# Kernel tuning notes

Hardware: AMD Instinct MI355X
Metric: run time of the kernel (lower is better)

Reference implementation:

```python
import jax, jax.numpy as jnp
import numpy as np

B, D = 4096, 128
LU, LI = 10, 20
NU, NI = 100000, 100000
NFU, NFI = 2000, 5000
MARGIN = 1.0


def setup_inputs() -> dict:
    key = jax.random.key(0)
    ks = jax.random.split(key, 32)
    s = 0.05
    n = lambda i, shape: (jax.random.normal(ks[i], shape, dtype=jnp.float32) * s)
    inp = {
        'user_indices': jax.random.randint(ks[0], (B,), 0, NU),
        'user_feat': jax.random.randint(ks[1], (B, LU), 0, NFU),
        'pos_item_indices': jax.random.randint(ks[2], (B,), 0, NI),
        'pos_item_feat': jax.random.randint(ks[3], (B, LI), 0, NFI),
        'neg_item_indices': jax.random.randint(ks[4], (B, 1), 0, NI),
        'neg_item_feat': jax.random.randint(ks[5], (B, 1, LI), 0, NFI),
        'comp_neg_indices': jax.random.randint(ks[6], (B,), 0, NI),
        'eps': jax.random.normal(ks[7], (B, D), dtype=jnp.float32),
        # learned parameters
        'emb_user': n(8, (NU, D)),
        'emb_item': n(9, (NI, D)),
        'emb_feat_user': n(10, (NFU, D)).at[0].set(0.0),  # row 0 is padding
        'emb_feat_item': n(11, (NFI, D)).at[0].set(0.0),
        'pop_emb_user': n(12, (D,)),
        'int_emb_user': n(13, (D,)),
        'pop_emb_item': n(14, (D,)),
        'int_emb_item': n(15, (D,)),
        'W_pop': n(16, (D, D)), 'b_pop': jnp.zeros((D,), jnp.float32),
        'W_int': n(17, (D, D)), 'b_int': jnp.zeros((D,), jnp.float32),
        'enc_W': n(18, (LI * D, D)), 'enc_b': jnp.zeros((D,), jnp.float32),
        'dec_W': n(19, (D, LI * D)), 'dec_b': jnp.zeros((LI * D,), jnp.float32),
        'fc11_W': n(20, (D, D)), 'fc11_b': jnp.zeros((D,), jnp.float32),
        'fc12_W': n(21, (D, D)), 'fc12_b': jnp.zeros((D,), jnp.float32),
    }
    return inp


def _attend_pool(fuse, feat_mask, vec, W, b):
    # fuse: [B, L+1, D], feat_mask: [B, L+1] (int, 0 = padded)
    scores = jnp.einsum('bld,d->bl', fuse, vec)
    scores = jnp.where(feat_mask == 0, -jnp.inf, scores)
    w = jax.nn.softmax(scores, axis=1)
    pooled = jnp.einsum('bld,bl->bd', fuse, w)
    return pooled @ W + b


def _branch(idx, feat, emb_table, feat_table, pop_vec, int_vec, W_pop, b_pop, W_int, b_int):
    e = emb_table[idx]                       # [B, D]
    fe = feat_table[feat]                    # [B, L, D]
    fuse = jnp.concatenate([e[:, None, :], fe], axis=1)           # [B, L+1, D]
    ones = jnp.ones((idx.shape[0], 1), dtype=feat.dtype)
    mask = jnp.concatenate([ones, feat], axis=1)                  # [B, L+1]
    hot = _attend_pool(fuse, mask, pop_vec, W_pop, b_pop)
    cold = _attend_pool(fuse, mask, int_vec, W_int, b_int)
    return hot, cold, e, fe


def reference(user_indices, user_feat, pos_item_indices, pos_item_feat,
              neg_item_indices, neg_item_feat, comp_neg_indices, eps,
              emb_user, emb_item, emb_feat_user, emb_feat_item,
              pop_emb_user, int_emb_user, pop_emb_item, int_emb_item,
              W_pop, b_pop, W_int, b_int,
              enc_W, enc_b, dec_W, dec_b, fc11_W, fc11_b, fc12_W, fc12_b):
    neg_item_indices = neg_item_indices.squeeze(1)
    neg_item_feat = neg_item_feat.squeeze(1)

    u_hot, u_cold, _, _ = _branch(user_indices, user_feat, emb_user, emb_feat_user,
                                  pop_emb_user, int_emb_user, W_pop, b_pop, W_int, b_int)
    p_hot, p_cold, pos_e, pos_fe = _branch(pos_item_indices, pos_item_feat, emb_item, emb_feat_item,
                                           pop_emb_item, int_emb_item, W_pop, b_pop, W_int, b_int)
    n_hot, n_cold, _, _ = _branch(neg_item_indices, neg_item_feat, emb_item, emb_feat_item,
                                  pop_emb_item, int_emb_item, W_pop, b_pop, W_int, b_int)

    loss_hot = jax.nn.relu(jnp.sum((u_hot - p_hot) ** 2, -1)
                           - jnp.sum((u_hot - n_hot) ** 2, -1) + MARGIN)
    loss_cold = jax.nn.relu(jnp.sum((u_cold - p_cold) ** 2, -1)
                            - jnp.sum((u_cold - n_cold) ** 2, -1) + MARGIN)

    # VAE over positive item feature embeddings
    x = pos_fe.reshape(pos_fe.shape[0], LI * D)
    h1 = jax.nn.relu(x @ enc_W + enc_b)
    mu = h1 @ fc11_W + fc11_b
    logvar = h1 @ fc12_W + fc12_b
    z = eps * jnp.exp(0.5 * logvar) + mu
    recon = z @ dec_W + dec_b                                    # [B, LI*D]
    mse = jnp.sum((recon - x) ** 2)
    kld = -0.5 * jnp.sum(1.0 + logvar - mu ** 2 - jnp.exp(logvar))
    vae_l = mse / LI + kld

    comp_e = emb_item[comp_neg_indices]
    mmi = -jnp.sum(jax.nn.log_sigmoid(jnp.sum(z * pos_e, 1) - jnp.sum(z * comp_e, 1)))
    item_vae_loss = mmi + vae_l + jnp.sum((z - pos_e) ** 2)

    return loss_hot, loss_cold, item_vae_loss
```

## Files before the change

kernel.cpp:

```cpp
#include <hip/hip_runtime.h>
#include <math.h>

#define BATCH 4096
#define DIM 128
#define LU 10
#define LI 20

typedef float  f32x4  __attribute__((ext_vector_type(4)));
typedef short  s16x8  __attribute__((ext_vector_type(8)));

__device__ __forceinline__ short f2bf(float x) {
    unsigned u = __float_as_uint(x);
    u += 0x7FFFu + ((u >> 16) & 1u);
    return (short)(u >> 16);
}

__global__ __launch_bounds__(256) void k_prep(
    const float* __restrict__ enc_W, const float* __restrict__ dec_W,
    const float* __restrict__ fc11_W, const float* __restrict__ fc12_W,
    const float* __restrict__ W_pop, const float* __restrict__ W_int,
    const float* __restrict__ ef_item, const float* __restrict__ ef_user,
    short* __restrict__ encWT, short* __restrict__ decWT,
    short* __restrict__ fc11WT, short* __restrict__ fc12WT,
    short* __restrict__ wpopT, short* __restrict__ wintT,
    short* __restrict__ ef16, short* __restrict__ efU16)
{
    __shared__ float tile[32][33];
    const int b = blockIdx.x;
    const int t = threadIdx.x;

    if (b < 704) {
        const float* src; short* dst; int r0, c0, src_ld, dst_ld;
        if (b < 320) {
            int tk = b % 80, tj = b / 80;
            src = enc_W; dst = encWT; r0 = tk * 32; c0 = tj * 32; src_ld = 128; dst_ld = 2560;
        } else if (b < 640) {
            int tb = b - 320; int tc = tb % 80, td = tb / 80;
            src = dec_W; dst = decWT; r0 = td * 32; c0 = tc * 32; src_ld = 2560; dst_ld = 128;
        } else if (b < 656) {
            int tb = b - 640; int tk = tb % 4, tj = tb / 4;
            src = fc11_W; dst = fc11WT; r0 = tk * 32; c0 = tj * 32; src_ld = 128; dst_ld = 128;
        } else if (b < 672) {
            int tb = b - 656; int tk = tb % 4, tj = tb / 4;
            src = fc12_W; dst = fc12WT; r0 = tk * 32; c0 = tj * 32; src_ld = 128; dst_ld = 128;
        } else if (b < 688) {
            int tb = b - 672; int tk = tb % 4, tj = tb / 4;
            src = W_pop; dst = wpopT; r0 = tk * 32; c0 = tj * 32; src_ld = 128; dst_ld = 128;
        } else {
            int tb = b - 688; int tk = tb % 4, tj = tb / 4;
            src = W_int; dst = wintT; r0 = tk * 32; c0 = tj * 32; src_ld = 128; dst_ld = 128;
        }
        for (int q = 0; q < 4; ++q) {
            int e = t + q * 256;
            int r = e >> 5, c = e & 31;
            tile[r][c] = src[(size_t)(r0 + r) * src_ld + (c0 + c)];
        }
        __syncthreads();
        for (int q = 0; q < 4; ++q) {
            int e = t + q * 256;
            int r = e >> 5, c = e & 31;
            dst[(size_t)(c0 + r) * dst_ld + (r0 + c)] = f2bf(tile[c][r]);
        }
    } else if (b < 1329) {
        int base = (b - 704) * 1024 + t * 4;
        float4 v = *(const float4*)(ef_item + base);
        short4 o;
        o.x = f2bf(v.x); o.y = f2bf(v.y); o.z = f2bf(v.z); o.w = f2bf(v.w);
        *(short4*)(ef16 + base) = o;
    } else {
        int base = (b - 1329) * 1024 + t * 4;
        float4 v = *(const float4*)(ef_user + base);
        short4 o;
        o.x = f2bf(v.x); o.y = f2bf(v.y); o.z = f2bf(v.z); o.w = f2bf(v.w);
        *(short4*)(efU16 + base) = o;
    }
}

template<int L>
__device__ __forceinline__ void pool_1p(
    const int* __restrict__ idxp, const int* __restrict__ featp,
    const float* __restrict__ etab, const unsigned short* __restrict__ ftab16,
    const float* __restrict__ vpop, const float* __restrict__ vint,
    float* __restrict__ poolH, float* __restrict__ poolC,
    int i_in, int lane)
{
    const int i = __builtin_amdgcn_readfirstlane(i_in);
    const int d = lane * 2;
    const float2 vp = *(const float2*)(vpop + d);
    const float2 vi = *(const float2*)(vint + d);

    int fidx[L];
#pragma unroll
    for (int l = 0; l < L; ++l) fidx[l] = featp[i * L + l];
    const int idx0 = idxp[i];

    const float2 e0 = *(const float2*)(etab + (size_t)idx0 * DIM + d);
    unsigned rr[L];
#pragma unroll
    for (int l = 0; l < L; ++l)
        rr[l] = *(const unsigned*)(ftab16 + (size_t)fidx[l] * DIM + d);

    unsigned mbits = 1u;
#pragma unroll
    for (int l = 0; l < L; ++l) mbits |= (fidx[l] != 0 ? 2u : 0u) << l;

    float sp[L + 1], si[L + 1];
    sp[0] = e0.x * vp.x + e0.y * vp.y;
    si[0] = e0.x * vi.x + e0.y * vi.y;
#pragma unroll
    for (int l = 0; l < L; ++l) {
        float x = __uint_as_float(rr[l] << 16);
        float y = __uint_as_float(rr[l] & 0xFFFF0000u);
        sp[l + 1] = x * vp.x + y * vp.y;
        si[l + 1] = x * vi.x + y * vi.y;
    }

#pragma unroll
    for (int l = 0; l <= L; ++l) {
        float a = sp[l], b = si[l];
        a += __shfl_xor(a, 1, 64);  b += __shfl_xor(b, 1, 64);
        a += __shfl_xor(a, 2, 64);  b += __shfl_xor(b, 2, 64);
        a += __shfl_xor(a, 4, 64);  b += __shfl_xor(b, 4, 64);
        a += __shfl_xor(a, 8, 64);  b += __shfl_xor(b, 8, 64);
        a += __shfl_xor(a, 16, 64); b += __shfl_xor(b, 16, 64);
        a += __shfl_xor(a, 32, 64); b += __shfl_xor(b, 32, 64);
        sp[l] = a; si[l] = b;
    }

    float mh = sp[0], mc = si[0];
#pragma unroll
    for (int l = 1; l <= L; ++l) {
        bool v = (mbits >> l) & 1u;
        mh = v ? fmaxf(mh, sp[l]) : mh;
        mc = v ? fmaxf(mc, si[l]) : mc;
    }
    float sh = 0.f, sc = 0.f;
#pragma unroll
    for (int l = 0; l <= L; ++l) {
        bool v = (l == 0) | ((mbits >> l) & 1u);
        float eh = v ? __expf(sp[l] - mh) : 0.f;
        float ec = v ? __expf(si[l] - mc) : 0.f;
        sp[l] = eh; si[l] = ec;
        sh += eh; sc += ec;
    }
    const float rh = 1.f / sh, rc = 1.f / sc;

    float hx = sp[0] * e0.x, hy = sp[0] * e0.y;
    float cx = si[0] * e0.x, cy = si[0] * e0.y;
#pragma unroll
    for (int l = 0; l < L; ++l) {
        float x = __uint_as_float(rr[l] << 16);
        float y = __uint_as_float(rr[l] & 0xFFFF0000u);
        hx += sp[l + 1] * x; hy += sp[l + 1] * y;
        cx += si[l + 1] * x; cy += si[l + 1] * y;
    }
    float2 oH; oH.x = hx * rh; oH.y = hy * rh;
    float2 oC; oC.x = cx * rc; oC.y = cy * rc;
    *(float2*)(poolH + (size_t)i * DIM + d) = oH;
    *(float2*)(poolC + (size_t)i * DIM + d) = oC;
}

__global__ __launch_bounds__(256) void k_AB(
    const int* __restrict__ user_idx, const int* __restrict__ user_feat,
    const int* __restrict__ pos_idx,  const int* __restrict__ pos_feat,
    const int* __restrict__ neg_idx,  const int* __restrict__ neg_feat,
    const int* __restrict__ comp_idx,
    const float* __restrict__ emb_user, const float* __restrict__ emb_item,
    const float* __restrict__ pop_u, const float* __restrict__ int_u,
    const float* __restrict__ pop_i, const float* __restrict__ int_i,
    const float* __restrict__ eps,
    const float* __restrict__ enc_b,
    const float* __restrict__ fc11_b, const float* __restrict__ fc12_b,
    const short* __restrict__ encWT,
    const short* __restrict__ fc11WT, const short* __restrict__ fc12WT,
    const short* __restrict__ ef16, const short* __restrict__ efU16,
    float* __restrict__ pooled,
    short* __restrict__ zbuf, float* __restrict__ vae_part)
{
    __shared__ int   featsL[320];
    __shared__ int   spi[16], sci[16];
    __shared__ __align__(16) short hlds[2048];
    __shared__ float sdots[4][16][3];
    __shared__ float red[256];

    const int t    = threadIdx.x;
    const int w    = t >> 6;
    const int lane = t & 63;
    const int g    = lane >> 4;
    const int q    = lane & 15;
    const size_t SEC = (size_t)BATCH * DIM;

    if (blockIdx.x >= 256) {
        const int pb = blockIdx.x - 256;
        const int br = pb % 3;
        const int i  = (pb / 3) * 4 + w;
        if (br == 0) {
            pool_1p<LU>(user_idx, user_feat, emb_user,
                        (const unsigned short*)efU16, pop_u, int_u,
                        pooled + 0 * SEC, pooled + 1 * SEC, i, lane);
        } else if (br == 1) {
            pool_1p<LI>(pos_idx, pos_feat, emb_item,
                        (const unsigned short*)ef16, pop_i, int_i,
                        pooled + 2 * SEC, pooled + 3 * SEC, i, lane);
        } else {
            pool_1p<LI>(neg_idx, neg_feat, emb_item,
                        (const unsigned short*)ef16, pop_i, int_i,
                        pooled + 4 * SEC, pooled + 5 * SEC, i, lane);
        }
        return;
    }

    const int sg = blockIdx.x;
    const int i0 = sg * 16;

    if (t < 16)      spi[t] = pos_idx[i0 + t];
    else if (t < 32) sci[t - 16] = comp_idx[i0 + t - 16];
    if (t < 256) featsL[t] = pos_feat[i0 * LI + t];
    if (t < 64)  featsL[256 + t] = pos_feat[i0 * LI + 256 + t];
    __syncthreads();

    const int j0 = w * 32 + q;
    const int j1 = j0 + 16;
    const short* bbase0 = encWT + (size_t)j0 * 2560 + g * 8;
    const short* bbase1 = encWT + (size_t)j1 * 2560 + g * 8;

    f32x4 acc0 = {0.f, 0.f, 0.f, 0.f};
    f32x4 acc1 = {0.f, 0.f, 0.f, 0.f};
    for (int l = 0; l < LI; ++l) {
        const int f = featsL[q * LI + l];
        const short* arow = ef16 + (size_t)f * DIM + g * 8;
#pragma unroll
        for (int dt = 0; dt < 4; ++dt) {
            const int koff = l * 128 + dt * 32;
            s16x8 a  = *(const s16x8*)(arow + dt * 32);
            s16x8 b0 = *(const s16x8*)(bbase0 + koff);
            s16x8 b1 = *(const s16x8*)(bbase1 + koff);
            acc0 = __builtin_amdgcn_mfma_f32_16x16x32_bf16(a, b0, acc0, 0, 0, 0);
            acc1 = __builtin_amdgcn_mfma_f32_16x16x32_bf16(a, b1, acc1, 0, 0, 0);
        }
    }

    {
        float eb0 = enc_b[j0], eb1 = enc_b[j1];
#pragma unroll
        for (int r = 0; r < 4; ++r) {
            int s = g * 4 + r;
            float h0 = acc0[r] + eb0; h0 = h0 > 0.f ? h0 : 0.f;
            float h1 = acc1[r] + eb1; h1 = h1 > 0.f ? h1 : 0.f;
            int swz = (s & 7) << 3;
            hlds[(s * 128 + j0) ^ swz] = f2bf(h0);
            hlds[(s * 128 + j1) ^ swz] = f2bf(h1);
        }
    }
    __syncthreads();

    const short* fb0_11 = fc11WT + (size_t)j0 * DIM + g * 8;
    const short* fb1_11 = fc11WT + (size_t)j1 * DIM + g * 8;
    const short* fb0_12 = fc12WT + (size_t)j0 * DIM + g * 8;
    const short* fb1_12 = fc12WT + (size_t)j1 * DIM + g * 8;

    f32x4 mu0 = {0.f,0.f,0.f,0.f}, mu1 = {0.f,0.f,0.f,0.f};
    f32x4 lv0 = {0.f,0.f,0.f,0.f}, lv1 = {0.f,0.f,0.f,0.f};
#pragma unroll
    for (int kt = 0; kt < 4; ++kt) {
        int sidx = (q * 128 + kt * 32 + g * 8) ^ ((q & 7) << 3);
        s16x8 a = *(const s16x8*)&hlds[sidx];
        s16x8 w11a = *(const s16x8*)(fb0_11 + kt * 32);
        s16x8 w11b = *(const s16x8*)(fb1_11 + kt * 32);
        s16x8 w12a = *(const s16x8*)(fb0_12 + kt * 32);
        s16x8 w12b = *(const s16x8*)(fb1_12 + kt * 32);
        mu0 = __builtin_amdgcn_mfma_f32_16x16x32_bf16(a, w11a, mu0, 0, 0, 0);
        mu1 = __builtin_amdgcn_mfma_f32_16x16x32_bf16(a, w11b, mu1, 0, 0, 0);
        lv0 = __builtin_amdgcn_mfma_f32_16x16x32_bf16(a, w12a, lv0, 0, 0, 0);
        lv1 = __builtin_amdgcn_mfma_f32_16x16x32_bf16(a, w12b, lv1, 0, 0, 0);
    }

    float b11_0 = fc11_b[j0], b11_1 = fc11_b[j1];
    float b12_0 = fc12_b[j0], b12_1 = fc12_b[j1];

    float kacc = 0.f;
#pragma unroll
    for (int r = 0; r < 4; ++r) {
        const int s = g * 4 + r;
        const int i = i0 + s;
        float m0 = mu0[r] + b11_0, m1 = mu1[r] + b11_1;
        float v0 = lv0[r] + b12_0, v1 = lv1[r] + b12_1;
        float e0 = eps[(size_t)i * DIM + j0];
        float e1 = eps[(size_t)i * DIM + j1];
        float z0 = e0 * expf(0.5f * v0) + m0;
        float z1 = e1 * expf(0.5f * v1) + m1;
        zbuf[(size_t)i * DIM + j0] = f2bf(z0);
        zbuf[(size_t)i * DIM + j1] = f2bf(z1);
        kacc += (1.f + v0 - m0 * m0 - expf(v0)) + (1.f + v1 - m1 * m1 - expf(v1));

        const size_t pb2 = (size_t)spi[s] * DIM;
        const size_t cb2 = (size_t)sci[s] * DIM;
        float pe0 = emb_item[pb2 + j0], pe1 = emb_item[pb2 + j1];
        float ce0 = emb_item[cb2 + j0], ce1 = emb_item[cb2 + j1];
        float zp = z0 * pe0 + z1 * pe1;
        float zc = z0 * ce0 + z1 * ce1;
        float d0 = z0 - pe0, d1 = z1 - pe1;
        float zq = d0 * d0 + d1 * d1;
        for (int mm = 8; mm >= 1; mm >>= 1) {
            zp += __shfl_xor(zp, mm, 64);
            zc += __shfl_xor(zc, mm, 64);
            zq += __shfl_xor(zq, mm, 64);
        }
        if (q == 0) {
            sdots[w][s][0] = zp;
            sdots[w][s][1] = zc;
            sdots[w][s][2] = zq;
        }
    }

    red[t] = -0.5f * kacc;
    __syncthreads();
    if (t < 16) {
        float zp = 0.f, zc = 0.f, zq = 0.f;
        for (int ww = 0; ww < 4; ++ww) {
            zp += sdots[ww][t][0];
            zc += sdots[ww][t][1];
            zq += sdots[ww][t][2];
        }
        float x = zp - zc;
        float ls = (x >= 0.f) ? -log1pf(expf(-x)) : (x - log1pf(expf(x)));
        red[t] += -ls + zq;
    }
    __syncthreads();
    for (int off = 128; off > 0; off >>= 1) {
        if (t < off) red[t] += red[t + off];
        __syncthreads();
    }
    if (t == 0) vae_part[sg] = red[0];
}

__global__ __launch_bounds__(256) void k_C(
    const float* __restrict__ pooled,
    const short* __restrict__ wpopT, const short* __restrict__ wintT,
    const int* __restrict__ pos_feat,
    const float* __restrict__ ef_item, const float* __restrict__ dec_b,
    const short* __restrict__ decWT, const short* __restrict__ zbuf,
    float* __restrict__ out_hot, float* __restrict__ out_cold,
    float* __restrict__ dec_part)
{
    __shared__ int   featsL[320];
    __shared__ float red[256];
    __shared__ float sArr[4][16];

    const int t    = threadIdx.x;
    const int w    = t >> 6;
    const int lane = t & 63;
    const int g    = lane >> 4;
    const int q    = lane & 15;

    if (blockIdx.x >= 2048) {
        const int i0 = (blockIdx.x - 2048) * 16;
        const int h     = w >> 1;
        const int other = (w & 1) + 1;
        const float* pu = pooled + (size_t)(0 * 2 + h) * BATCH * DIM;
        const float* po = pooled + (size_t)(other * 2 + h) * BATCH * DIM;
        const short* wT = h ? wintT : wpopT;

        s16x8 afr[4];
#pragma unroll
        for (int kt = 0; kt < 4; ++kt) {
            const size_t off = (size_t)(i0 + q) * DIM + kt * 32 + g * 8;
            f32x4 ua = *(const f32x4*)(pu + off);
            f32x4 ub = *(const f32x4*)(pu + off + 4);
            f32x4 oa = *(const f32x4*)(po + off);
            f32x4 ob = *(const f32x4*)(po + off + 4);
            s16x8 v;
            v[0] = f2bf(ua[0] - oa[0]); v[1] = f2bf(ua[1] - oa[1]);
            v[2] = f2bf(ua[2] - oa[2]); v[3] = f2bf(ua[3] - oa[3]);
            v[4] = f2bf(ub[0] - ob[0]); v[5] = f2bf(ub[1] - ob[1]);
            v[6] = f2bf(ub[2] - ob[2]); v[7] = f2bf(ub[3] - ob[3]);
            afr[kt] = v;
        }

        float sq0 = 0.f, sq1 = 0.f, sq2 = 0.f, sq3 = 0.f;
        for (int fr = 0; fr < 8; ++fr) {
            const short* bb = wT + (size_t)(fr * 16 + q) * DIM + g * 8;
            f32x4 acc = {0.f, 0.f, 0.f, 0.f};
#pragma unroll
            for (int kt = 0; kt < 4; ++kt) {
                s16x8 bfr = *(const s16x8*)(bb + kt * 32);
                acc = __builtin_amdgcn_mfma_f32_16x16x32_bf16(afr[kt], bfr, acc, 0, 0, 0);
            }
            sq0 += acc[0] * acc[0]; sq1 += acc[1] * acc[1];
            sq2 += acc[2] * acc[2]; sq3 += acc[3] * acc[3];
        }
        for (int m = 8; m >= 1; m >>= 1) {
            sq0 += __shfl_xor(sq0, m, 64);
            sq1 += __shfl_xor(sq1, m, 64);
            sq2 += __shfl_xor(sq2, m, 64);
            sq3 += __shfl_xor(sq3, m, 64);
        }
        if (q == 0) {
            sArr[w][g * 4 + 0] = sq0;
            sArr[w][g * 4 + 1] = sq1;
            sArr[w][g * 4 + 2] = sq2;
            sArr[w][g * 4 + 3] = sq3;
        }
        __syncthreads();
        if (t < 16) {
            float v = sArr[0][t] - sArr[1][t] + 1.0f;
            out_hot[i0 + t] = v > 0.f ? v : 0.f;
        } else if (t < 32) {
            int s = t - 16;
            float v = sArr[2][s] - sArr[3][s] + 1.0f;
            out_cold[i0 + s] = v > 0.f ? v : 0.f;
        }
        return;
    }

    const int db     = blockIdx.x;
    const int cchunk = db >> 8;
    const int sb     = db & 255;
    const int i0     = sb * 16;

    if (t < 256) featsL[t] = pos_feat[i0 * LI + t];
    if (t < 64)  featsL[256 + t] = pos_feat[i0 * LI + 256 + t];
    __syncthreads();

    s16x8 za[4];
#pragma unroll
    for (int kt = 0; kt < 4; ++kt)
        za[kt] = *(const s16x8*)(zbuf + (size_t)(i0 + q) * DIM + kt * 32 + g * 8);

    const int cw = cchunk * 320 + w * 80;

    s16x8 bb[5][4];
    float xs[5][4];
    float bias[5];
#pragma unroll
    for (int fp = 0; fp < 5; ++fp) {
        const int c = cw + fp * 16 + q;
        const short* bp = decWT + (size_t)c * DIM + g * 8;
#pragma unroll
        for (int kt = 0; kt < 4; ++kt)
            bb[fp][kt] = *(const s16x8*)(bp + kt * 32);
        const int l = c >> 7, dcol = c & 127;
#pragma unroll
        for (int r = 0; r < 4; ++r)
            xs[fp][r] = ef_item[(size_t)featsL[(g * 4 + r) * LI + l] * DIM + dcol];
        bias[fp] = dec_b[c];
    }

    float macc = 0.f;
#pragma unroll
    for (int fp = 0; fp < 5; ++fp) {
        f32x4 acc = {0.f, 0.f, 0.f, 0.f};
#pragma unroll
        for (int kt = 0; kt < 4; ++kt)
            acc = __builtin_amdgcn_mfma_f32_16x16x32_bf16(za[kt], bb[fp][kt], acc, 0, 0, 0);
#pragma unroll
        for (int r = 0; r < 4; ++r) {
            float dd = acc[r] + bias[fp] - xs[fp][r];
            macc += dd * dd;
        }
    }

    red[t] = macc;
    __syncthreads();
    for (int off = 128; off > 0; off >>= 1) {
        if (t < off) red[t] += red[t + off];
        __syncthreads();
    }
    if (t == 0) dec_part[db] = red[0];
}

__global__ __launch_bounds__(256) void k_E(
    const float* __restrict__ vae_part, const float* __restrict__ dec_part,
    float* __restrict__ out_scalar)
{
    __shared__ float red[256];
    const int t = threadIdx.x;
    float b3 = 0.f;
    for (int qq = t; qq < 2048; qq += 256) b3 += dec_part[qq];
    red[t] = vae_part[t] + 0.05f * b3;
    __syncthreads();
    for (int off = 128; off > 0; off >>= 1) {
        if (t < off) red[t] += red[t + off];
        __syncthreads();
    }
    if (t == 0) out_scalar[0] = red[0];
}

extern "C" void kernel_launch(void* const* d_in, const int* in_sizes, int n_in,
                              void* d_out, int out_size, void* d_ws, size_t ws_size,
                              hipStream_t stream) {
    const int*   user_idx  = (const int*)d_in[0];
    const int*   user_feat = (const int*)d_in[1];
    const int*   pos_idx   = (const int*)d_in[2];
    const int*   pos_feat  = (const int*)d_in[3];
    const int*   neg_idx   = (const int*)d_in[4];
    const int*   neg_feat  = (const int*)d_in[5];
    const int*   comp_idx  = (const int*)d_in[6];
    const float* eps       = (const float*)d_in[7];
    const float* emb_user  = (const float*)d_in[8];
    const float* emb_item  = (const float*)d_in[9];
    const float* ef_user   = (const float*)d_in[10];
    const float* ef_item   = (const float*)d_in[11];
    const float* pop_u     = (const float*)d_in[12];
    const float* int_u     = (const float*)d_in[13];
    const float* pop_i     = (const float*)d_in[14];
    const float* int_i     = (const float*)d_in[15];
    const float* W_pop     = (const float*)d_in[16];
    const float* W_int     = (const float*)d_in[18];
    const float* enc_W     = (const float*)d_in[20];
    const float* enc_b     = (const float*)d_in[21];
    const float* dec_W     = (const float*)d_in[22];
    const float* dec_b     = (const float*)d_in[23];
    const float* fc11_W    = (const float*)d_in[24];
    const float* fc11_b    = (const float*)d_in[25];
    const float* fc12_W    = (const float*)d_in[26];
    const float* fc12_b    = (const float*)d_in[27];

    float* out = (float*)d_out;
    char*  ws  = (char*)d_ws;

    short* encWT    = (short*)(ws);
    short* decWT    = (short*)(ws + 655360);
    short* fc11WT   = (short*)(ws + 1310720);
    short* fc12WT   = (short*)(ws + 1343488);
    short* wpopT    = (short*)(ws + 1376256);
    short* wintT    = (short*)(ws + 1409024);
    short* ef16     = (short*)(ws + 1441792);
    short* efU16    = (short*)(ws + 2721792);
    short* zbuf     = (short*)(ws + 3233792);
    float* pooled   = (float*)(ws + 4282368);
    float* vae_part = (float*)(ws + 16865280);
    float* dec_part = (float*)(ws + 16866304);

    k_prep<<<dim3(1579), dim3(256), 0, stream>>>(
        enc_W, dec_W, fc11_W, fc12_W, W_pop, W_int, ef_item, ef_user,
        encWT, decWT, fc11WT, fc12WT, wpopT, wintT, ef16, efU16);

    k_AB<<<dim3(3328), dim3(256), 0, stream>>>(
        user_idx, user_feat, pos_idx, pos_feat, neg_idx, neg_feat, comp_idx,
        emb_user, emb_item,
        pop_u, int_u, pop_i, int_i,
        eps, enc_b, fc11_b, fc12_b,
        encWT, fc11WT, fc12WT, ef16, efU16,
        pooled, zbuf, vae_part);

    k_C<<<dim3(2304), dim3(256), 0, stream>>>(
        pooled, wpopT, wintT, pos_feat, ef_item, dec_b, decWT, zbuf,
        out, out + BATCH, dec_part);

    k_E<<<dim3(1), dim3(256), 0, stream>>>(vae_part, dec_part, out + 2 * BATCH);
}
```

Baseline: 90.91 us.

## Precompute per-feature attention scores in prep kernel and gather them in pooling

Adds blocks to the prep kernel that compute the dot product of every feature-table row with the pop and int attention vectors and store them as scalar tables. The pooling routine then gathers these precomputed scores per feature instead of computing per-lane products followed by a 6-step shuffle reduction for each of the L+1 slots. Only the slot for the main embedding still needs the in-wave reduction. This moves the work to 7000 table rows, which is comparable to the 12288 pooled samples, and adds 875 prep blocks plus scattered scalar gathers in exchange for far fewer cross-lane shuffles.

```diff
diff --git a/kernel.cpp b/kernel.cpp
--- a/kernel.cpp
+++ b/kernel.cpp
@@ -20,10 +20,14 @@
     const float* __restrict__ fc11_W, const float* __restrict__ fc12_W,
     const float* __restrict__ W_pop, const float* __restrict__ W_int,
     const float* __restrict__ ef_item, const float* __restrict__ ef_user,
+    const float* __restrict__ pop_i, const float* __restrict__ int_i,
+    const float* __restrict__ pop_u, const float* __restrict__ int_u,
     short* __restrict__ encWT, short* __restrict__ decWT,
     short* __restrict__ fc11WT, short* __restrict__ fc12WT,
     short* __restrict__ wpopT, short* __restrict__ wintT,
-    short* __restrict__ ef16, short* __restrict__ efU16)
+    short* __restrict__ ef16, short* __restrict__ efU16,
+    float* __restrict__ projIP, float* __restrict__ projII,
+    float* __restrict__ projUP, float* __restrict__ projUI)
 {
     __shared__ float tile[32][33];
     const int b = blockIdx.x;
@@ -67,27 +71,49 @@
         short4 o;
         o.x = f2bf(v.x); o.y = f2bf(v.y); o.z = f2bf(v.z); o.w = f2bf(v.w);
         *(short4*)(ef16 + base) = o;
-    } else {
+    } else if (b < 1579) {
         int base = (b - 1329) * 1024 + t * 4;
         float4 v = *(const float4*)(ef_user + base);
         short4 o;
         o.x = f2bf(v.x); o.y = f2bf(v.y); o.z = f2bf(v.z); o.w = f2bf(v.w);
         *(short4*)(efU16 + base) = o;
+    } else {
+        const int pb = b - 1579;
+        const float* tab; const float* v0p; const float* v1p;
+        float* o0; float* o1; int row;
+        if (pb < 625) {
+            row = pb * 8 + (t >> 5);
+            tab = ef_item; v0p = pop_i; v1p = int_i; o0 = projIP; o1 = projII;
+        } else {
+            row = (pb - 625) * 8 + (t >> 5);
+            tab = ef_user; v0p = pop_u; v1p = int_u; o0 = projUP; o1 = projUI;
+        }
+        const int d = (t & 31) * 4;
+        float4 rv = *(const float4*)(tab + (size_t)row * DIM + d);
+        float4 a  = *(const float4*)(v0p + d);
+        float4 c  = *(const float4*)(v1p + d);
+        float s0 = rv.x * a.x + rv.y * a.y + rv.z * a.z + rv.w * a.w;
+        float s1 = rv.x * c.x + rv.y * c.y + rv.z * c.z + rv.w * c.w;
+        s0 += __shfl_xor(s0, 1, 64);  s1 += __shfl_xor(s1, 1, 64);
+        s0 += __shfl_xor(s0, 2, 64);  s1 += __shfl_xor(s1, 2, 64);
+        s0 += __shfl_xor(s0, 4, 64);  s1 += __shfl_xor(s1, 4, 64);
+        s0 += __shfl_xor(s0, 8, 64);  s1 += __shfl_xor(s1, 8, 64);
+        s0 += __shfl_xor(s0, 16, 64); s1 += __shfl_xor(s1, 16, 64);
+        if ((t & 31) == 0) { o0[row] = s0; o1[row] = s1; }
     }
 }
 
 template<int L>
-__device__ __forceinline__ void pool_1p(
+__device__ __forceinline__ void pool_sc(
     const int* __restrict__ idxp, const int* __restrict__ featp,
     const float* __restrict__ etab, const unsigned short* __restrict__ ftab16,
+    const float* __restrict__ projP, const float* __restrict__ projI,
     const float* __restrict__ vpop, const float* __restrict__ vint,
     float* __restrict__ poolH, float* __restrict__ poolC,
     int i_in, int lane)
 {
     const int i = __builtin_amdgcn_readfirstlane(i_in);
     const int d = lane * 2;
-    const float2 vp = *(const float2*)(vpop + d);
-    const float2 vi = *(const float2*)(vint + d);
 
     int fidx[L];
 #pragma unroll
@@ -100,32 +126,30 @@
     for (int l = 0; l < L; ++l)
         rr[l] = *(const unsigned*)(ftab16 + (size_t)fidx[l] * DIM + d);
 
+    float sp[L + 1], si[L + 1];
+#pragma unroll
+    for (int l = 0; l < L; ++l) {
+        sp[l + 1] = projP[fidx[l]];
+        si[l + 1] = projI[fidx[l]];
+    }
+
+    {
+        const float2 vp = *(const float2*)(vpop + d);
+        const float2 vi = *(const float2*)(vint + d);
+        float aH = e0.x * vp.x + e0.y * vp.y;
+        float aC = e0.x * vi.x + e0.y * vi.y;
+        aH += __shfl_xor(aH, 1, 64);  aC += __shfl_xor(aC, 1, 64);
+        aH += __shfl_xor(aH, 2, 64);  aC += __shfl_xor(aC, 2, 64);
+        aH += __shfl_xor(aH, 4, 64);  aC += __shfl_xor(aC, 4, 64);
+        aH += __shfl_xor(aH, 8, 64);  aC += __shfl_xor(aC, 8, 64);
+        aH += __shfl_xor(aH, 16, 64); aC += __shfl_xor(aC, 16, 64);
+        aH += __shfl_xor(aH, 32, 64); aC += __shfl_xor(aC, 32, 64);
+        sp[0] = aH; si[0] = aC;
+    }
+
     unsigned mbits = 1u;
 #pragma unroll
     for (int l = 0; l < L; ++l) mbits |= (fidx[l] != 0 ? 2u : 0u) << l;
-
-    float sp[L + 1], si[L + 1];
-    sp[0] = e0.x * vp.x + e0.y * vp.y;
-    si[0] = e0.x * vi.x + e0.y * vi.y;
-#pragma unroll
-    for (int l = 0; l < L; ++l) {
-        float x = __uint_as_float(rr[l] << 16);
-        float y = __uint_as_float(rr[l] & 0xFFFF0000u);
-        sp[l + 1] = x * vp.x + y * vp.y;
-        si[l + 1] = x * vi.x + y * vi.y;
-    }
-
-#pragma unroll
-    for (int l = 0; l <= L; ++l) {
-        float a = sp[l], b = si[l];
-        a += __shfl_xor(a, 1, 64);  b += __shfl_xor(b, 1, 64);
-        a += __shfl_xor(a, 2, 64);  b += __shfl_xor(b, 2, 64);
-        a += __shfl_xor(a, 4, 64);  b += __shfl_xor(b, 4, 64);
-        a += __shfl_xor(a, 8, 64);  b += __shfl_xor(b, 8, 64);
-        a += __shfl_xor(a, 16, 64); b += __shfl_xor(b, 16, 64);
-        a += __shfl_xor(a, 32, 64); b += __shfl_xor(b, 32, 64);
-        sp[l] = a; si[l] = b;
-    }
 
     float mh = sp[0], mc = si[0];
 #pragma unroll
@@ -174,6 +198,8 @@
     const short* __restrict__ encWT,
     const short* __restrict__ fc11WT, const short* __restrict__ fc12WT,
     const short* __restrict__ ef16, const short* __restrict__ efU16,
+    const float* __restrict__ projIP, const float* __restrict__ projII,
+    const float* __restrict__ projUP, const float* __restrict__ projUI,
     float* __restrict__ pooled,
     short* __restrict__ zbuf, float* __restrict__ vae_part)
 {
@@ -195,16 +221,19 @@
         const int br = pb % 3;
         const int i  = (pb / 3) * 4 + w;
         if (br == 0) {
-            pool_1p<LU>(user_idx, user_feat, emb_user,
-                        (const unsigned short*)efU16, pop_u, int_u,
+            pool_sc<LU>(user_idx, user_feat, emb_user,
+                        (const unsigned short*)efU16, projUP, projUI,
+                        pop_u, int_u,
                         pooled + 0 * SEC, pooled + 1 * SEC, i, lane);
         } else if (br == 1) {
-            pool_1p<LI>(pos_idx, pos_feat, emb_item,
-                        (const unsigned short*)ef16, pop_i, int_i,
+            pool_sc<LI>(pos_idx, pos_feat, emb_item,
+                        (const unsigned short*)ef16, projIP, projII,
+                        pop_i, int_i,
                         pooled + 2 * SEC, pooled + 3 * SEC, i, lane);
         } else {
-            pool_1p<LI>(neg_idx, neg_feat, emb_item,
-                        (const unsigned short*)ef16, pop_i, int_i,
+            pool_sc<LI>(neg_idx, neg_feat, emb_item,
+                        (const unsigned short*)ef16, projIP, projII,
+                        pop_i, int_i,
                         pooled + 4 * SEC, pooled + 5 * SEC, i, lane);
         }
         return;
@@ -531,10 +560,16 @@
     float* pooled   = (float*)(ws + 4282368);
     float* vae_part = (float*)(ws + 16865280);
     float* dec_part = (float*)(ws + 16866304);
-
-    k_prep<<<dim3(1579), dim3(256), 0, stream>>>(
+    float* projIP   = (float*)(ws + 16874496);
+    float* projII   = (float*)(ws + 16894496);
+    float* projUP   = (float*)(ws + 16914496);
+    float* projUI   = (float*)(ws + 16922496);
+
+    k_prep<<<dim3(2454), dim3(256), 0, stream>>>(
         enc_W, dec_W, fc11_W, fc12_W, W_pop, W_int, ef_item, ef_user,
-        encWT, decWT, fc11WT, fc12WT, wpopT, wintT, ef16, efU16);
+        pop_i, int_i, pop_u, int_u,
+        encWT, decWT, fc11WT, fc12WT, wpopT, wintT, ef16, efU16,
+        projIP, projII, projUP, projUI);
 
     k_AB<<<dim3(3328), dim3(256), 0, stream>>>(
         user_idx, user_feat, pos_idx, pos_feat, neg_idx, neg_feat, comp_idx,
@@ -542,6 +577,7 @@
         pop_u, int_u, pop_i, int_i,
         eps, enc_b, fc11_b, fc12_b,
         encWT, fc11WT, fc12WT, ef16, efU16,
+        projIP, projII, projUP, projUI,
         pooled, zbuf, vae_part);
 
     k_C<<<dim3(2304), dim3(256), 0, stream>>>(
```

After: 88.33 us. -2.8%, faster.
